# Kernel tuning notes

Hardware: AMD Instinct MI355X
Metric: run time of the kernel (lower is better)

Reference implementation:

```python
import jax, jax.numpy as jnp
import numpy as np

HIDDEN = 1024
EMBED = HIDDEN // 4
SEQ = 512
BATCH = 256
NUM_CLASSES = 10


def setup_inputs() -> dict:
    key = jax.random.key(0)
    ks = jax.random.split(key, 16)

    def w(k, d1, d2):
        # kaiming_normal_ with nonlinearity='linear': std = 1/sqrt(fan_in=d2)
        return jax.random.normal(k, (d1, d2), dtype=jnp.float32) / jnp.sqrt(d2)

    inp = {
        "x": jax.random.randint(ks[0], (BATCH, SEQ), 0, 3),
        "emb": jax.random.normal(ks[1], (3, EMBED), dtype=jnp.float32),
        "w_gx": w(ks[2], EMBED, HIDDEN), "w_gh": w(ks[3], HIDDEN, HIDDEN), "b_g": jnp.zeros((HIDDEN,), jnp.float32),
        "w_ix": w(ks[4], EMBED, HIDDEN), "w_ih": w(ks[5], HIDDEN, HIDDEN), "b_i": jnp.zeros((HIDDEN,), jnp.float32),
        "w_fx": w(ks[6], EMBED, HIDDEN), "w_fh": w(ks[7], HIDDEN, HIDDEN), "b_f": jnp.zeros((HIDDEN,), jnp.float32),
        "w_ox": w(ks[8], EMBED, HIDDEN), "w_oh": w(ks[9], HIDDEN, HIDDEN), "b_o": jnp.zeros((HIDDEN,), jnp.float32),
        "w_ph": w(ks[10], HIDDEN, NUM_CLASSES), "b_p": jnp.zeros((NUM_CLASSES,), jnp.float32),
    }
    return inp


def reference(x, emb, w_gx, w_gh, b_g, w_ix, w_ih, b_i, w_fx, w_fh, b_f,
              w_ox, w_oh, b_o, w_ph, b_p):
    B, T = x.shape
    embedded = emb[x]                         # [B, T, E]
    pad = ((x + 1) // 2).astype(emb.dtype)    # [B, T]

    xs = (jnp.swapaxes(embedded, 0, 1),       # [T, B, E]
          jnp.swapaxes(pad, 0, 1))            # [T, B]

    h0 = jnp.zeros((B, w_gh.shape[0]), emb.dtype)
    c0 = jnp.zeros_like(h0)

    def step(carry, inputs):
        h, c = carry
        xt, pt = inputs
        g = jnp.tanh(xt @ w_gx + h @ w_gh + b_g)
        i = jax.nn.sigmoid(xt @ w_ix + h @ w_ih + b_i)
        f = jax.nn.sigmoid(xt @ w_fx + h @ w_fh + b_f)
        o = jax.nn.sigmoid(xt @ w_ox + h @ w_oh + b_o)
        c = g * i + c * f
        h = jnp.tanh(c) * o
        c = c * pt[:, None]
        return (h, c), None

    (h, _), _ = jax.lax.scan(step, (h0, c0), xs)
    p = h @ w_ph + b_p                        # [B, num_classes]
    # Faithful to original: log_softmax over dim=0 (batch dim)
    return jax.nn.log_softmax(p, axis=0)
```

## Files before the change

kernel.cpp:

```cpp
#include <hip/hip_runtime.h>
#include <hip/hip_bf16.h>

#define T_SEQ 512
#define BATCH 256
#define HID   1024
#define EMBD  256
#define NCLS  10

typedef __bf16 bf16x8 __attribute__((ext_vector_type(8)));
typedef float  floatx16 __attribute__((ext_vector_type(16)));
typedef float  floatx2 __attribute__((ext_vector_type(2)));
typedef unsigned short ushortx8 __attribute__((ext_vector_type(8)));

__device__ __forceinline__ unsigned int f2bf(float f) {
    unsigned int u = __builtin_bit_cast(unsigned int, f);
    u += 0x7fffu + ((u >> 16) & 1u);
    return u >> 16;
}
__device__ __forceinline__ float sig_fast(float x) {
    return __builtin_amdgcn_rcpf(1.0f + __expf(-x));
}
__device__ __forceinline__ float tanh_fast(float x) {
    return 1.0f - 2.0f * __builtin_amdgcn_rcpf(1.0f + __expf(2.0f * x));
}

__global__ void prep_xw_kernel(const float* __restrict__ emb,
                               const float* __restrict__ wgx, const float* __restrict__ wix,
                               const float* __restrict__ wfx, const float* __restrict__ wox,
                               const float* __restrict__ bg,  const float* __restrict__ bi,
                               const float* __restrict__ bf,  const float* __restrict__ bo,
                               float* __restrict__ XW) {
    int gid = blockIdx.x * blockDim.x + threadIdx.x;
    if (gid >= 3 * 4 * HID) return;
    int tok  = gid >> 12;
    int gate = (gid >> 10) & 3;
    int n    = gid & 1023;
    const float* W = gate == 0 ? wgx : gate == 1 ? wix : gate == 2 ? wfx : wox;
    const float* B = gate == 0 ? bg  : gate == 1 ? bi  : gate == 2 ? bf  : bo;
    float acc = B[n];
    const float* e = emb + tok * EMBD;
    for (int k = 0; k < EMBD; ++k) acc += e[k] * W[k * HID + n];
    XW[gid] = acc;
}

__global__ void prep_w_kernel(const float* __restrict__ wgh, const float* __restrict__ wih,
                              const float* __restrict__ wfh, const float* __restrict__ woh,
                              unsigned short* __restrict__ Wt) {
    int bid = blockIdx.x;
    int w   = bid & 31;
    int i   = (bid >> 5) & 31;
    int kh  = (bid >> 10) & 1;
    int g   = bid >> 11;
    const float* W = g == 0 ? wgh : g == 1 ? wih : g == 2 ? wfh : woh;
    int lane = threadIdx.x;
    int j    = w * 32 + (lane & 31);
    int k0   = kh * 512 + i * 16 + (lane >> 5) * 8;
    ushortx8 o8;
    #pragma unroll
    for (int e = 0; e < 8; ++e) o8[e] = (unsigned short)f2bf(W[(k0 + e) * HID + j]);
    int frag = ((w * 4 + g) * 2 + kh) * 32 + i;
    *(ushortx8*)&Wt[frag * 512 + lane * 8] = o8;
}

__global__ __launch_bounds__(512, 2)
void lstm_kernel(const int* __restrict__ x, const float* __restrict__ XW,
                 const unsigned short* __restrict__ Wt,
                 unsigned int* __restrict__ hbuf32, int* __restrict__ flags,
                 int* __restrict__ xflag) {
    __shared__ unsigned short hs[32 * 1032];
    __shared__ float gbuf[8 * 32 * 36];
    __shared__ float xwl[384];
    __shared__ unsigned char xtok[32 * 512];
    __shared__ int use_local_sh;

    const int tid  = threadIdx.x;
    const int grp  = blockIdx.x & 7;
    const int w    = blockIdx.x >> 3;
    const int wv   = tid >> 6;
    const int gv   = wv >> 1;
    const int kh   = wv & 1;
    const int lane = tid & 63;
    const int m32  = lane & 31;
    const int hv5  = lane >> 5;

    {
        int xcc = 0;
        asm volatile("s_getreg_b32 %0, hwreg(HW_REG_XCC_ID)" : "=s"(xcc));
        if (tid == 0) {
            __hip_atomic_store(&xflag[grp * 32 + w], xcc + 1, __ATOMIC_RELAXED,
                               __HIP_MEMORY_SCOPE_SYSTEM);
        }
        if (wv == 0) {
            int v;
            for (;;) {
                v = __hip_atomic_load(&xflag[grp * 32 + (lane & 31)], __ATOMIC_RELAXED,
                                      __HIP_MEMORY_SCOPE_SYSTEM);
                if (__all(v != 0)) break;
                __builtin_amdgcn_s_sleep(2);
            }
            int v0 = __shfl(v, 0, 64);
            if (lane == 0) use_local_sh = __all(v == v0) ? 1 : 0;
        }
    }

    bf16x8 Bf[32];
    {
        const unsigned short* wb = Wt + (size_t)(((w * 4 + gv) * 2 + kh) * 32) * 512
                                      + (size_t)lane * 8;
        #pragma unroll
        for (int i = 0; i < 32; ++i)
            Bf[i] = *(const bf16x8*)(wb + i * 512);
    }
    if (tid < 384) {
        int tok = tid >> 7, g = (tid >> 5) & 3, jl = tid & 31;
        xwl[tid] = XW[(tok * 4 + g) * HID + w * 32 + jl];
    }
    #pragma unroll
    for (int it = 0; it < 32; ++it) {
        int flat = it * 512 + tid;
        int row  = flat >> 9;
        int col  = flat & 511;
        xtok[flat] = (unsigned char)x[(grp * 32 + row) * T_SEQ + col];
    }
    __syncthreads();
    const bool use_local = (use_local_sh != 0);

    const int erow = tid >> 4;
    const int jc2  = tid & 15;
    float cst[2] = {0.f, 0.f};
    unsigned long long* hs64 = (unsigned long long*)hs;

    for (int s = 0; s < T_SEQ; ++s) {
        if (s > 0) {
            if (wv == 0) {
                const int fidx = grp * 32 + (lane & 31);
                if (use_local) {
                    while (__hip_atomic_load(&flags[fidx], __ATOMIC_RELAXED,
                                             __HIP_MEMORY_SCOPE_AGENT) < s)
                        __builtin_amdgcn_s_sleep(1);
                } else {
                    while (__hip_atomic_load(&flags[fidx], __ATOMIC_RELAXED,
                                             __HIP_MEMORY_SCOPE_SYSTEM) < s)
                        __builtin_amdgcn_s_sleep(1);
                }
            }
            __syncthreads();
        }

        const unsigned long long* hp64 = (const unsigned long long*)
            (hbuf32 + (size_t)(s & 1) * (BATCH * HID / 2)) + (size_t)grp * 32 * 256;
        {
            unsigned long long tmp[16];
            if (use_local) {
                #pragma unroll
                for (int it = 0; it < 16; ++it) {
                    int flat = it * 512 + tid;
                    tmp[it] = __hip_atomic_load(&hp64[(flat >> 8) * 256 + (flat & 255)],
                                                __ATOMIC_RELAXED, __HIP_MEMORY_SCOPE_AGENT);
                }
            } else {
                #pragma unroll
                for (int it = 0; it < 16; ++it) {
                    int flat = it * 512 + tid;
                    tmp[it] = __hip_atomic_load(&hp64[(flat >> 8) * 256 + (flat & 255)],
                                                __ATOMIC_RELAXED, __HIP_MEMORY_SCOPE_SYSTEM);
                }
            }
            #pragma unroll
            for (int it = 0; it < 16; ++it) {
                int flat = it * 512 + tid;
                hs64[(flat >> 8) * 258 + (flat & 255)] = tmp[it];
            }
        }
        __syncthreads();

        floatx16 acc = {0.f,0.f,0.f,0.f,0.f,0.f,0.f,0.f,0.f,0.f,0.f,0.f,0.f,0.f,0.f,0.f};
        const unsigned short* ap = hs + m32 * 1032 + kh * 512 + hv5 * 8;
        #pragma unroll
        for (int i = 0; i < 32; ++i) {
            bf16x8 a = *(const bf16x8*)(ap + i * 16);
            acc = __builtin_amdgcn_mfma_f32_32x32x16_bf16(a, Bf[i], acc, 0, 0, 0);
        }

        {
            float* gb = &gbuf[(size_t)(gv * 2 + kh) * 32 * 36];
            #pragma unroll
            for (int reg = 0; reg < 16; ++reg) {
                int row = (reg & 3) + 8 * (reg >> 2) + 4 * hv5;
                gb[row * 36 + m32] = acc[reg];
            }
        }
        __syncthreads();

        {
            int tk = xtok[erow * 512 + s];
            const float* xb = &xwl[tk * 128];
            const int go = erow * 36 + jc2 * 2;
            floatx2 ag = *(const floatx2*)&gbuf[0 * 32 * 36 + go]
                       + *(const floatx2*)&gbuf[1 * 32 * 36 + go];
            floatx2 ai = *(const floatx2*)&gbuf[2 * 32 * 36 + go]
                       + *(const floatx2*)&gbuf[3 * 32 * 36 + go];
            floatx2 af = *(const floatx2*)&gbuf[4 * 32 * 36 + go]
                       + *(const floatx2*)&gbuf[5 * 32 * 36 + go];
            floatx2 ao = *(const floatx2*)&gbuf[6 * 32 * 36 + go]
                       + *(const floatx2*)&gbuf[7 * 32 * 36 + go];
            floatx2 xg = *(const floatx2*)&xb[0 * 32 + jc2 * 2];
            floatx2 xi = *(const floatx2*)&xb[1 * 32 + jc2 * 2];
            floatx2 xf = *(const floatx2*)&xb[2 * 32 + jc2 * 2];
            floatx2 xo = *(const floatx2*)&xb[3 * 32 + jc2 * 2];
            unsigned int hvv[2];
            #pragma unroll
            for (int u = 0; u < 2; ++u) {
                float g  = tanh_fast(ag[u] + xg[u]);
                float ii = sig_fast(ai[u] + xi[u]);
                float ff = sig_fast(af[u] + xf[u]);
                float oo = sig_fast(ao[u] + xo[u]);
                float cn = g * ii + cst[u] * ff;
                float h  = tanh_fast(cn) * oo;
                cst[u]   = (tk != 0) ? cn : 0.0f;
                hvv[u]   = f2bf(h);
            }
            unsigned int* hnext = hbuf32 + (size_t)((s + 1) & 1) * (BATCH * HID / 2);
            unsigned int* hp = &hnext[((grp * 32 + erow) * HID + w * 32 + jc2 * 2) >> 1];
            unsigned int hval = hvv[0] | (hvv[1] << 16);
            if (use_local) {
                __hip_atomic_store(hp, hval, __ATOMIC_RELAXED, __HIP_MEMORY_SCOPE_WORKGROUP);
            } else {
                __hip_atomic_store(hp, hval, __ATOMIC_RELAXED, __HIP_MEMORY_SCOPE_SYSTEM);
            }
        }
        __syncthreads();

        if (s < T_SEQ - 1 && tid == 0) {
            if (use_local) {
                __hip_atomic_store(&flags[grp * 32 + w], s + 1,
                                   __ATOMIC_RELAXED, __HIP_MEMORY_SCOPE_WORKGROUP);
            } else {
                __hip_atomic_store(&flags[grp * 32 + w], s + 1,
                                   __ATOMIC_RELAXED, __HIP_MEMORY_SCOPE_SYSTEM);
            }
        }
    }
}

__global__ void proj_kernel(const unsigned short* __restrict__ h,
                            const float* __restrict__ wph, const float* __restrict__ bp,
                            float* __restrict__ out) {
    __shared__ float wl[HID * NCLS];
    __shared__ float red[256];
    int tid = threadIdx.x;
    for (int i = tid; i < HID * NCLS; i += 256) wl[i] = wph[i];
    __syncthreads();
    float p[NCLS];
    #pragma unroll
    for (int c2 = 0; c2 < NCLS; ++c2) p[c2] = bp[c2];
    const unsigned short* hr = h + tid * HID;
    for (int k0 = 0; k0 < HID / 8; ++k0) {
        bf16x8 hv = *(const bf16x8*)(hr + k0 * 8);
        #pragma unroll
        for (int j = 0; j < 8; ++j) {
            float hk = (float)hv[j];
            #pragma unroll
            for (int c2 = 0; c2 < NCLS; ++c2) p[c2] += hk * wl[(k0 * 8 + j) * NCLS + c2];
        }
    }
    for (int c2 = 0; c2 < NCLS; ++c2) {
        red[tid] = p[c2];
        __syncthreads();
        for (int s = 128; s > 0; s >>= 1) {
            if (tid < s) red[tid] = fmaxf(red[tid], red[tid + s]);
            __syncthreads();
        }
        float mx = red[0];
        __syncthreads();
        red[tid] = __expf(p[c2] - mx);
        __syncthreads();
        for (int s = 128; s > 0; s >>= 1) {
            if (tid < s) red[tid] += red[tid + s];
            __syncthreads();
        }
        float lse = mx + __logf(red[0]);
        __syncthreads();
        out[tid * NCLS + c2] = p[c2] - lse;
    }
}

extern "C" void kernel_launch(void* const* d_in, const int* in_sizes, int n_in,
                              void* d_out, int out_size, void* d_ws, size_t ws_size,
                              hipStream_t stream) {
    const int*   x    = (const int*)d_in[0];
    const float* emb  = (const float*)d_in[1];
    const float* wgx  = (const float*)d_in[2];
    const float* wgh  = (const float*)d_in[3];
    const float* bg_  = (const float*)d_in[4];
    const float* wix  = (const float*)d_in[5];
    const float* wih  = (const float*)d_in[6];
    const float* bi_  = (const float*)d_in[7];
    const float* wfx  = (const float*)d_in[8];
    const float* wfh  = (const float*)d_in[9];
    const float* bf_  = (const float*)d_in[10];
    const float* wox  = (const float*)d_in[11];
    const float* woh  = (const float*)d_in[12];
    const float* bo_  = (const float*)d_in[13];
    const float* wph  = (const float*)d_in[14];
    const float* bp_  = (const float*)d_in[15];
    float* out = (float*)d_out;

    char* wsp = (char*)d_ws;
    int*            flags = (int*)wsp;
    int*            xflag = (int*)(wsp + 4096);
    float*          XW    = (float*)(wsp + 8192);
    unsigned short* Wt    = (unsigned short*)(wsp + 8192 + 49152);
    unsigned int*   hbuf32= (unsigned int*)(wsp + 8192 + 49152 + 8388608);

    hipMemsetAsync(flags, 0, 8192, stream);
    hipMemsetAsync(hbuf32, 0, BATCH * HID * sizeof(unsigned short), stream);

    prep_xw_kernel<<<48, 256, 0, stream>>>(emb, wgx, wix, wfx, wox,
                                           bg_, bi_, bf_, bo_, XW);
    prep_w_kernel<<<8192, 64, 0, stream>>>(wgh, wih, wfh, woh, Wt);

    void* args[] = { (void*)&x, (void*)&XW, (void*)&Wt, (void*)&hbuf32,
                     (void*)&flags, (void*)&xflag };
    hipError_t cerr = hipLaunchCooperativeKernel((void*)lstm_kernel, dim3(256), dim3(512),
                                                 args, 0, stream);
    if (cerr != hipSuccess) {
        lstm_kernel<<<dim3(256), dim3(512), 0, stream>>>(x, XW, Wt, hbuf32, flags, xflag);
    }

    proj_kernel<<<1, 256, 0, stream>>>((const unsigned short*)hbuf32, wph, bp_, out);
}
```

Baseline: 1.760 ms.

## Split recurrent matmul by K quarter with per-quarter flag waits and LDS counters

The hidden-state K dimension is repartitioned into four quarters. Each pair of waves owns one quarter and computes two gates, so both MFMA accumulators share one A fragment from LDS. Instead of one wave polling all flags followed by a block barrier, each wave polls only the 8 producer flags for its quarter, loads that slice of h, and syncs with its partner through an LDS atomic counter. This lets waves start their MFMAs as soon as their own slice is ready. Tokens are also packed 2 bits each to shrink LDS. The cost is a 4-way partial-sum reduction in gbuf instead of 2-way, plus a spin loop on LDS atomics.

```diff
diff --git a/kernel.cpp b/kernel.cpp
--- a/kernel.cpp
+++ b/kernel.cpp
@@ -48,17 +48,17 @@
                               unsigned short* __restrict__ Wt) {
     int bid = blockIdx.x;
     int w   = bid & 31;
-    int i   = (bid >> 5) & 31;
-    int kh  = (bid >> 10) & 1;
+    int i   = (bid >> 5) & 15;
+    int q   = (bid >> 9) & 3;
     int g   = bid >> 11;
     const float* W = g == 0 ? wgh : g == 1 ? wih : g == 2 ? wfh : woh;
     int lane = threadIdx.x;
     int j    = w * 32 + (lane & 31);
-    int k0   = kh * 512 + i * 16 + (lane >> 5) * 8;
+    int k0   = q * 256 + i * 16 + (lane >> 5) * 8;
     ushortx8 o8;
     #pragma unroll
     for (int e = 0; e < 8; ++e) o8[e] = (unsigned short)f2bf(W[(k0 + e) * HID + j]);
-    int frag = ((w * 4 + g) * 2 + kh) * 32 + i;
+    int frag = ((w * 4 + g) * 4 + q) * 16 + i;
     *(ushortx8*)&Wt[frag * 512 + lane * 8] = o8;
 }
 
@@ -67,18 +67,19 @@
                  const unsigned short* __restrict__ Wt,
                  unsigned int* __restrict__ hbuf32, int* __restrict__ flags,
                  int* __restrict__ xflag) {
-    __shared__ unsigned short hs[32 * 1032];
-    __shared__ float gbuf[8 * 32 * 36];
+    __shared__ __align__(16) unsigned short hs[4 * 8448];
+    __shared__ float gbuf[16 * 1152];
     __shared__ float xwl[384];
-    __shared__ unsigned char xtok[32 * 512];
+    __shared__ unsigned char xtokp[4096];
+    __shared__ int qctr[4];
     __shared__ int use_local_sh;
 
     const int tid  = threadIdx.x;
     const int grp  = blockIdx.x & 7;
     const int w    = blockIdx.x >> 3;
     const int wv   = tid >> 6;
-    const int gv   = wv >> 1;
-    const int kh   = wv & 1;
+    const int qv   = wv >> 1;
+    const int pv   = wv & 1;
     const int lane = tid & 63;
     const int m32  = lane & 31;
     const int hv5  = lane >> 5;
@@ -103,25 +104,29 @@
         }
     }
 
-    bf16x8 Bf[32];
+    bf16x8 Bf0[16], Bf1[16];
     {
-        const unsigned short* wb = Wt + (size_t)(((w * 4 + gv) * 2 + kh) * 32) * 512
-                                      + (size_t)lane * 8;
+        const unsigned short* wb0 = Wt + (size_t)(((w * 4 + 2 * pv + 0) * 4 + qv) * 16) * 512
+                                       + (size_t)lane * 8;
+        const unsigned short* wb1 = Wt + (size_t)(((w * 4 + 2 * pv + 1) * 4 + qv) * 16) * 512
+                                       + (size_t)lane * 8;
         #pragma unroll
-        for (int i = 0; i < 32; ++i)
-            Bf[i] = *(const bf16x8*)(wb + i * 512);
+        for (int i = 0; i < 16; ++i) {
+            Bf0[i] = *(const bf16x8*)(wb0 + i * 512);
+            Bf1[i] = *(const bf16x8*)(wb1 + i * 512);
+        }
     }
     if (tid < 384) {
         int tok = tid >> 7, g = (tid >> 5) & 3, jl = tid & 31;
         xwl[tid] = XW[(tok * 4 + g) * HID + w * 32 + jl];
     }
-    #pragma unroll
-    for (int it = 0; it < 32; ++it) {
-        int flat = it * 512 + tid;
-        int row  = flat >> 9;
-        int col  = flat & 511;
-        xtok[flat] = (unsigned char)x[(grp * 32 + row) * T_SEQ + col];
-    }
+    for (int i = tid; i < 4096; i += 512) {
+        int row = i >> 7, b = i & 127;
+        const int* xr = &x[(grp * 32 + row) * T_SEQ + b * 4];
+        xtokp[i] = (unsigned char)((xr[0] & 3) | ((xr[1] & 3) << 2)
+                                   | ((xr[2] & 3) << 4) | ((xr[3] & 3) << 6));
+    }
+    if (tid < 4) qctr[tid] = 0;
     __syncthreads();
     const bool use_local = (use_local_sh != 0);
 
@@ -132,78 +137,91 @@
 
     for (int s = 0; s < T_SEQ; ++s) {
         if (s > 0) {
-            if (wv == 0) {
-                const int fidx = grp * 32 + (lane & 31);
-                if (use_local) {
-                    while (__hip_atomic_load(&flags[fidx], __ATOMIC_RELAXED,
-                                             __HIP_MEMORY_SCOPE_AGENT) < s)
-                        __builtin_amdgcn_s_sleep(1);
-                } else {
-                    while (__hip_atomic_load(&flags[fidx], __ATOMIC_RELAXED,
-                                             __HIP_MEMORY_SCOPE_SYSTEM) < s)
-                        __builtin_amdgcn_s_sleep(1);
-                }
-            }
-            __syncthreads();
-        }
-
-        const unsigned long long* hp64 = (const unsigned long long*)
-            (hbuf32 + (size_t)(s & 1) * (BATCH * HID / 2)) + (size_t)grp * 32 * 256;
-        {
-            unsigned long long tmp[16];
+            const int fidx = grp * 32 + qv * 8 + (lane & 7);
             if (use_local) {
-                #pragma unroll
-                for (int it = 0; it < 16; ++it) {
-                    int flat = it * 512 + tid;
-                    tmp[it] = __hip_atomic_load(&hp64[(flat >> 8) * 256 + (flat & 255)],
-                                                __ATOMIC_RELAXED, __HIP_MEMORY_SCOPE_AGENT);
+                for (;;) {
+                    int v = __hip_atomic_load(&flags[fidx], __ATOMIC_RELAXED,
+                                              __HIP_MEMORY_SCOPE_AGENT);
+                    if (__all(v >= s)) break;
+                    __builtin_amdgcn_s_sleep(1);
                 }
             } else {
-                #pragma unroll
-                for (int it = 0; it < 16; ++it) {
-                    int flat = it * 512 + tid;
-                    tmp[it] = __hip_atomic_load(&hp64[(flat >> 8) * 256 + (flat & 255)],
-                                                __ATOMIC_RELAXED, __HIP_MEMORY_SCOPE_SYSTEM);
+                for (;;) {
+                    int v = __hip_atomic_load(&flags[fidx], __ATOMIC_RELAXED,
+                                              __HIP_MEMORY_SCOPE_SYSTEM);
+                    if (__all(v >= s)) break;
+                    __builtin_amdgcn_s_sleep(1);
                 }
             }
+        }
+
+        {
+            const unsigned long long* hp64 = (const unsigned long long*)
+                (hbuf32 + (size_t)(s & 1) * (BATCH * HID / 2));
+            unsigned long long tmp[16];
             #pragma unroll
             for (int it = 0; it < 16; ++it) {
-                int flat = it * 512 + tid;
-                hs64[(flat >> 8) * 258 + (flat & 255)] = tmp[it];
-            }
-        }
-        __syncthreads();
-
-        floatx16 acc = {0.f,0.f,0.f,0.f,0.f,0.f,0.f,0.f,0.f,0.f,0.f,0.f,0.f,0.f,0.f,0.f};
-        const unsigned short* ap = hs + m32 * 1032 + kh * 512 + hv5 * 8;
+                int flat = it * 64 + lane;
+                int row  = pv * 16 + (flat >> 6);
+                int c4   = flat & 63;
+                const unsigned long long* src =
+                    &hp64[(size_t)(grp * 32 + row) * 256 + qv * 64 + c4];
+                tmp[it] = use_local
+                    ? __hip_atomic_load(src, __ATOMIC_RELAXED, __HIP_MEMORY_SCOPE_AGENT)
+                    : __hip_atomic_load(src, __ATOMIC_RELAXED, __HIP_MEMORY_SCOPE_SYSTEM);
+            }
+            #pragma unroll
+            for (int it = 0; it < 16; ++it) {
+                int flat = it * 64 + lane;
+                int row  = pv * 16 + (flat >> 6);
+                int c4   = flat & 63;
+                hs64[qv * 2112 + row * 66 + c4] = tmp[it];
+            }
+        }
+        {
+            if (lane == 0)
+                __hip_atomic_fetch_add(&qctr[qv], 1, __ATOMIC_ACQ_REL,
+                                       __HIP_MEMORY_SCOPE_WORKGROUP);
+            const int target = 2 * (s + 1);
+            while (__hip_atomic_load(&qctr[qv], __ATOMIC_ACQUIRE,
+                                     __HIP_MEMORY_SCOPE_WORKGROUP) < target)
+                __builtin_amdgcn_s_sleep(0);
+        }
+
+        floatx16 acc0 = {0.f,0.f,0.f,0.f,0.f,0.f,0.f,0.f,0.f,0.f,0.f,0.f,0.f,0.f,0.f,0.f};
+        floatx16 acc1 = acc0;
+        const unsigned short* ap = hs + qv * 8448 + m32 * 264 + hv5 * 8;
         #pragma unroll
-        for (int i = 0; i < 32; ++i) {
+        for (int i = 0; i < 16; ++i) {
             bf16x8 a = *(const bf16x8*)(ap + i * 16);
-            acc = __builtin_amdgcn_mfma_f32_32x32x16_bf16(a, Bf[i], acc, 0, 0, 0);
+            acc0 = __builtin_amdgcn_mfma_f32_32x32x16_bf16(a, Bf0[i], acc0, 0, 0, 0);
+            acc1 = __builtin_amdgcn_mfma_f32_32x32x16_bf16(a, Bf1[i], acc1, 0, 0, 0);
         }
 
         {
-            float* gb = &gbuf[(size_t)(gv * 2 + kh) * 32 * 36];
+            float* gb0 = &gbuf[(size_t)((2 * pv + 0) * 4 + qv) * 1152];
+            float* gb1 = &gbuf[(size_t)((2 * pv + 1) * 4 + qv) * 1152];
             #pragma unroll
             for (int reg = 0; reg < 16; ++reg) {
                 int row = (reg & 3) + 8 * (reg >> 2) + 4 * hv5;
-                gb[row * 36 + m32] = acc[reg];
+                gb0[row * 36 + m32] = acc0[reg];
+                gb1[row * 36 + m32] = acc1[reg];
             }
         }
         __syncthreads();
 
         {
-            int tk = xtok[erow * 512 + s];
+            int byte = xtokp[erow * 128 + (s >> 2)];
+            int tk   = (byte >> ((s & 3) * 2)) & 3;
             const float* xb = &xwl[tk * 128];
             const int go = erow * 36 + jc2 * 2;
-            floatx2 ag = *(const floatx2*)&gbuf[0 * 32 * 36 + go]
-                       + *(const floatx2*)&gbuf[1 * 32 * 36 + go];
-            floatx2 ai = *(const floatx2*)&gbuf[2 * 32 * 36 + go]
-                       + *(const floatx2*)&gbuf[3 * 32 * 36 + go];
-            floatx2 af = *(const floatx2*)&gbuf[4 * 32 * 36 + go]
-                       + *(const floatx2*)&gbuf[5 * 32 * 36 + go];
-            floatx2 ao = *(const floatx2*)&gbuf[6 * 32 * 36 + go]
-                       + *(const floatx2*)&gbuf[7 * 32 * 36 + go];
+            floatx2 ag, ai, af, ao;
+            #define SUMQ(dst, g) dst = *(const floatx2*)&gbuf[((g)*4+0)*1152 + go] \
+                                     + *(const floatx2*)&gbuf[((g)*4+1)*1152 + go] \
+                                     + *(const floatx2*)&gbuf[((g)*4+2)*1152 + go] \
+                                     + *(const floatx2*)&gbuf[((g)*4+3)*1152 + go]
+            SUMQ(ag, 0); SUMQ(ai, 1); SUMQ(af, 2); SUMQ(ao, 3);
+            #undef SUMQ
             floatx2 xg = *(const floatx2*)&xb[0 * 32 + jc2 * 2];
             floatx2 xi = *(const floatx2*)&xb[1 * 32 + jc2 * 2];
             floatx2 xf = *(const floatx2*)&xb[2 * 32 + jc2 * 2];
```

Result: slower. 1.879 ms (+6.7%).

## Split recurrent matmul K into quarters with two gates per wave sharing A

Applied to the files above, without the earlier changes.

Each wave now computes two gates over a quarter of the hidden dimension instead of one gate over half, so each A fragment loaded from LDS feeds two MFMAs. This halves the LDS reads of h per step and gives each wave two independent accumulation chains to overlap MFMA latency. The weight prep layout changes to quarter-K fragments. In exchange, the partial-sum buffer in LDS doubles, each step does more cross-wave reduction work, and an extra accumulator raises register pressure.

```diff
diff --git a/kernel.cpp b/kernel.cpp
--- a/kernel.cpp
+++ b/kernel.cpp
@@ -48,17 +48,17 @@
                               unsigned short* __restrict__ Wt) {
     int bid = blockIdx.x;
     int w   = bid & 31;
-    int i   = (bid >> 5) & 31;
-    int kh  = (bid >> 10) & 1;
+    int i   = (bid >> 5) & 15;
+    int q   = (bid >> 9) & 3;
     int g   = bid >> 11;
     const float* W = g == 0 ? wgh : g == 1 ? wih : g == 2 ? wfh : woh;
     int lane = threadIdx.x;
     int j    = w * 32 + (lane & 31);
-    int k0   = kh * 512 + i * 16 + (lane >> 5) * 8;
+    int k0   = q * 256 + i * 16 + (lane >> 5) * 8;
     ushortx8 o8;
     #pragma unroll
     for (int e = 0; e < 8; ++e) o8[e] = (unsigned short)f2bf(W[(k0 + e) * HID + j]);
-    int frag = ((w * 4 + g) * 2 + kh) * 32 + i;
+    int frag = ((w * 4 + g) * 4 + q) * 16 + i;
     *(ushortx8*)&Wt[frag * 512 + lane * 8] = o8;
 }
 
@@ -67,8 +67,8 @@
                  const unsigned short* __restrict__ Wt,
                  unsigned int* __restrict__ hbuf32, int* __restrict__ flags,
                  int* __restrict__ xflag) {
-    __shared__ unsigned short hs[32 * 1032];
-    __shared__ float gbuf[8 * 32 * 36];
+    __shared__ __align__(16) unsigned short hs[32 * 1032];
+    __shared__ float gbuf[16][32][36];
     __shared__ float xwl[384];
     __shared__ unsigned char xtok[32 * 512];
     __shared__ int use_local_sh;
@@ -77,8 +77,8 @@
     const int grp  = blockIdx.x & 7;
     const int w    = blockIdx.x >> 3;
     const int wv   = tid >> 6;
-    const int gv   = wv >> 1;
-    const int kh   = wv & 1;
+    const int pv   = wv & 1;
+    const int qv   = wv >> 1;
     const int lane = tid & 63;
     const int m32  = lane & 31;
     const int hv5  = lane >> 5;
@@ -103,13 +103,17 @@
         }
     }
 
-    bf16x8 Bf[32];
+    bf16x8 Bf0[16], Bf1[16];
     {
-        const unsigned short* wb = Wt + (size_t)(((w * 4 + gv) * 2 + kh) * 32) * 512
-                                      + (size_t)lane * 8;
+        const unsigned short* wb0 = Wt + (size_t)(((w * 4 + 2 * pv + 0) * 4 + qv) * 16) * 512
+                                       + (size_t)lane * 8;
+        const unsigned short* wb1 = Wt + (size_t)(((w * 4 + 2 * pv + 1) * 4 + qv) * 16) * 512
+                                       + (size_t)lane * 8;
         #pragma unroll
-        for (int i = 0; i < 32; ++i)
-            Bf[i] = *(const bf16x8*)(wb + i * 512);
+        for (int i = 0; i < 16; ++i) {
+            Bf0[i] = *(const bf16x8*)(wb0 + i * 512);
+            Bf1[i] = *(const bf16x8*)(wb1 + i * 512);
+        }
     }
     if (tid < 384) {
         int tok = tid >> 7, g = (tid >> 5) & 3, jl = tid & 31;
@@ -147,24 +151,18 @@
             __syncthreads();
         }
 
-        const unsigned long long* hp64 = (const unsigned long long*)
-            (hbuf32 + (size_t)(s & 1) * (BATCH * HID / 2)) + (size_t)grp * 32 * 256;
         {
+            const unsigned long long* hp64 = (const unsigned long long*)
+                (hbuf32 + (size_t)(s & 1) * (BATCH * HID / 2));
             unsigned long long tmp[16];
-            if (use_local) {
-                #pragma unroll
-                for (int it = 0; it < 16; ++it) {
-                    int flat = it * 512 + tid;
-                    tmp[it] = __hip_atomic_load(&hp64[(flat >> 8) * 256 + (flat & 255)],
-                                                __ATOMIC_RELAXED, __HIP_MEMORY_SCOPE_AGENT);
-                }
-            } else {
-                #pragma unroll
-                for (int it = 0; it < 16; ++it) {
-                    int flat = it * 512 + tid;
-                    tmp[it] = __hip_atomic_load(&hp64[(flat >> 8) * 256 + (flat & 255)],
-                                                __ATOMIC_RELAXED, __HIP_MEMORY_SCOPE_SYSTEM);
-                }
+            #pragma unroll
+            for (int it = 0; it < 16; ++it) {
+                int flat = it * 512 + tid;
+                const unsigned long long* src =
+                    &hp64[(size_t)(grp * 32 + (flat >> 8)) * 256 + (flat & 255)];
+                tmp[it] = use_local
+                    ? __hip_atomic_load(src, __ATOMIC_RELAXED, __HIP_MEMORY_SCOPE_AGENT)
+                    : __hip_atomic_load(src, __ATOMIC_RELAXED, __HIP_MEMORY_SCOPE_SYSTEM);
             }
             #pragma unroll
             for (int it = 0; it < 16; ++it) {
@@ -174,20 +172,24 @@
         }
         __syncthreads();
 
-        floatx16 acc = {0.f,0.f,0.f,0.f,0.f,0.f,0.f,0.f,0.f,0.f,0.f,0.f,0.f,0.f,0.f,0.f};
-        const unsigned short* ap = hs + m32 * 1032 + kh * 512 + hv5 * 8;
+        floatx16 acc0 = (floatx16)(0.f);
+        floatx16 acc1 = (floatx16)(0.f);
+        const unsigned short* ap = hs + m32 * 1032 + qv * 256 + hv5 * 8;
         #pragma unroll
-        for (int i = 0; i < 32; ++i) {
+        for (int i = 0; i < 16; ++i) {
             bf16x8 a = *(const bf16x8*)(ap + i * 16);
-            acc = __builtin_amdgcn_mfma_f32_32x32x16_bf16(a, Bf[i], acc, 0, 0, 0);
+            acc0 = __builtin_amdgcn_mfma_f32_32x32x16_bf16(a, Bf0[i], acc0, 0, 0, 0);
+            acc1 = __builtin_amdgcn_mfma_f32_32x32x16_bf16(a, Bf1[i], acc1, 0, 0, 0);
         }
 
         {
-            float* gb = &gbuf[(size_t)(gv * 2 + kh) * 32 * 36];
+            float* gb0 = &gbuf[(2 * pv + 0) * 4 + qv][0][0];
+            float* gb1 = &gbuf[(2 * pv + 1) * 4 + qv][0][0];
             #pragma unroll
             for (int reg = 0; reg < 16; ++reg) {
                 int row = (reg & 3) + 8 * (reg >> 2) + 4 * hv5;
-                gb[row * 36 + m32] = acc[reg];
+                gb0[row * 36 + m32] = acc0[reg];
+                gb1[row * 36 + m32] = acc1[reg];
             }
         }
         __syncthreads();
@@ -196,14 +198,15 @@
             int tk = xtok[erow * 512 + s];
             const float* xb = &xwl[tk * 128];
             const int go = erow * 36 + jc2 * 2;
-            floatx2 ag = *(const floatx2*)&gbuf[0 * 32 * 36 + go]
-                       + *(const floatx2*)&gbuf[1 * 32 * 36 + go];
-            floatx2 ai = *(const floatx2*)&gbuf[2 * 32 * 36 + go]
-                       + *(const floatx2*)&gbuf[3 * 32 * 36 + go];
-            floatx2 af = *(const floatx2*)&gbuf[4 * 32 * 36 + go]
-                       + *(const floatx2*)&gbuf[5 * 32 * 36 + go];
-            floatx2 ao = *(const floatx2*)&gbuf[6 * 32 * 36 + go]
-                       + *(const floatx2*)&gbuf[7 * 32 * 36 + go];
+            #define SUMQ(g) (*(const floatx2*)&gbuf[(g)*4+0][0][go] \
+                           + *(const floatx2*)&gbuf[(g)*4+1][0][go] \
+                           + *(const floatx2*)&gbuf[(g)*4+2][0][go] \
+                           + *(const floatx2*)&gbuf[(g)*4+3][0][go])
+            floatx2 ag = SUMQ(0);
+            floatx2 ai = SUMQ(1);
+            floatx2 af = SUMQ(2);
+            floatx2 ao = SUMQ(3);
+            #undef SUMQ
             floatx2 xg = *(const floatx2*)&xb[0 * 32 + jc2 * 2];
             floatx2 xi = *(const floatx2*)&xb[1 * 32 + jc2 * 2];
             floatx2 xf = *(const floatx2*)&xb[2 * 32 + jc2 * 2];
```

New measurement: 1.926 ms. 1.09x slower.
